# Kernel optimization log

Measured on AMD Instinct MI355X. Metric: run time of the kernel, lower is better.

The kernel has to match this reference:

```python
import jax, jax.numpy as jnp
import numpy as np

DIM = 192
HEADS = 6
WIN = 7
N = WIN * WIN            # 49 tokens per window
NW = 64                  # windows per image
B = 64                   # images
BW = NW * B              # 4096 total windows
TABLE = (2 * WIN - 1) ** 2  # 169


def setup_inputs() -> dict:
    key = jax.random.key(0)
    ks = jax.random.split(key, 8)
    x = jax.random.normal(ks[0], (BW, N, DIM), dtype=jnp.float32)
    rpi = jax.random.randint(ks[1], (N, N), 0, TABLE, dtype=jnp.int64)
    # 0 / -100 additive mask (as in shifted-window attention)
    mask = jnp.where(jax.random.uniform(ks[2], (NW, N, N)) < 0.1, -100.0, 0.0).astype(jnp.float32)
    qkv_w = jax.random.normal(ks[3], (3 * DIM, DIM), dtype=jnp.float32) * 0.02
    qkv_b = jnp.zeros((3 * DIM,), dtype=jnp.float32)
    proj_w = jax.random.normal(ks[4], (DIM, DIM), dtype=jnp.float32) * 0.02
    proj_b = jnp.zeros((DIM,), dtype=jnp.float32)
    rpb_table = jax.random.normal(ks[5], (TABLE, HEADS), dtype=jnp.float32) * 0.02
    return {"x": x, "rpi": rpi, "mask": mask, "qkv_w": qkv_w, "qkv_b": qkv_b,
            "proj_w": proj_w, "proj_b": proj_b, "rpb_table": rpb_table}


def reference(x, rpi, mask, qkv_w, qkv_b, proj_w, proj_b, rpb_table):
    b_, n, c = x.shape
    hd = c // HEADS
    scale = hd ** -0.5
    qkv = (x @ qkv_w.T + qkv_b).reshape(b_, n, 3, HEADS, hd)
    qkv = jnp.transpose(qkv, (2, 0, 3, 1, 4))
    q, k, v = qkv[0], qkv[1], qkv[2]
    attn = jnp.einsum('bhnd,bhmd->bhnm', q * scale, k)  # [b_, h, n, n]
    # relative position bias gather: [n, n, h] -> [h, n, n]
    bias = rpb_table[rpi.reshape(-1)].reshape(n, n, HEADS)
    attn = attn + jnp.transpose(bias, (2, 0, 1))[None]
    # additive 0/-inf window mask
    nw = mask.shape[0]
    attn = attn.reshape(b_ // nw, nw, HEADS, n, n) + mask[None, :, None]
    attn = attn.reshape(-1, HEADS, n, n)
    attn = jax.nn.softmax(attn, axis=-1)
    out = jnp.einsum('bhnm,bhmd->bhnd', attn, v)
    out = jnp.transpose(out, (0, 2, 1, 3)).reshape(b_, n, c)
    out = out @ proj_w.T + proj_b
    return out
```

## Files before the change

### kernel.cpp

```cpp
#include <hip/hip_runtime.h>

#define DIM    192
#define HEADS  6
#define NTOK   49
#define NWIN   64

typedef __attribute__((ext_vector_type(8))) short short8;
typedef __attribute__((ext_vector_type(4))) float f32x4;

#define XS 200
#define VS 72
#define PS 72

#define USP_BYTES   26656
#define P_EOFF      9800
#define LDS_USHORTS ((USP_BYTES + 64 * XS * 2 + DIM * VS * 2) / 2)

#define BIAS_ELEMS (HEADS * NTOK * NTOK)
#define WQKV_SOFF   28864
#define WQKV_ELEMS  (3 * DIM * DIM)
#define WPROJ_SOFF  (WQKV_SOFF + WQKV_ELEMS)
#define WPROJ_ELEMS (DIM * DIM)
#define CMB_BOFF    ((size_t)(WPROJ_SOFF + WPROJ_ELEMS) * 2)
#define CMB2_ELEMS  (NWIN * HEADS * NTOK * 64)

__device__ __forceinline__ unsigned short f2bf(float f) {
    unsigned int u = __float_as_uint(f);
    u += 0x7FFFu + ((u >> 16) & 1u);
    return (unsigned short)(u >> 16);
}

__global__ void wa_prep_kernel(const int* __restrict__ rpi,
                               const float* __restrict__ rpb,
                               const float* __restrict__ qkv_w,
                               const float* __restrict__ proj_w,
                               const float* __restrict__ maskp,
                               float* __restrict__ bias,
                               unsigned short* __restrict__ wqkv,
                               unsigned short* __restrict__ wproj,
                               float* __restrict__ cmb2) {
    __shared__ int is64_s;
    if (threadIdx.x < 64) {
        int z = (rpi[2 * (int)threadIdx.x + 1] == 0) ? 1 : 0;
        unsigned long long b = __ballot(z);
        if (threadIdx.x == 0) is64_s = (__popcll(b) >= 48) ? 1 : 0;
    }
    __syncthreads();
    const int is64 = is64_s;
    const int base3 = BIAS_ELEMS + WQKV_ELEMS + WPROJ_ELEMS;
    const int total = base3 + (cmb2 ? CMB2_ELEMS : 0);
    for (int idx = blockIdx.x * blockDim.x + threadIdx.x; idx < total;
         idx += gridDim.x * blockDim.x) {
        if (idx < BIAS_ELEMS) {
            int h  = idx / (NTOK * NTOK);
            int nm = idx - h * (NTOK * NTOK);
            int r  = is64 ? rpi[2 * nm] : rpi[nm];
            bias[idx] = rpb[r * HEADS + h];
        } else if (idx < BIAS_ELEMS + WQKV_ELEMS) {
            int i = idx - BIAS_ELEMS;
            wqkv[i] = f2bf(qkv_w[i]);
        } else if (idx < base3) {
            int i = idx - BIAS_ELEMS - WQKV_ELEMS;
            wproj[i] = f2bf(proj_w[i]);
        } else {
            int i2  = idx - base3;
            int win = i2 / (HEADS * NTOK * 64);
            int rem = i2 - win * (HEADS * NTOK * 64);
            int h   = rem / (NTOK * 64);
            int rm2 = rem - h * (NTOK * 64);
            int q   = rm2 >> 6;
            int k   = rm2 & 63;
            float v = 0.f;
            if (k < NTOK) {
                int nm = q * NTOK + k;
                int r  = is64 ? rpi[2 * nm] : rpi[nm];
                v = rpb[r * HEADS + h] + maskp[win * (NTOK * NTOK) + nm];
            }
            cmb2[i2] = v;
        }
    }
}

template <bool CMB>
__global__ __launch_bounds__(512, 4)
void wa_attn_kernel(const float* __restrict__ x,
                    const float* __restrict__ maskp,
                    const unsigned short* __restrict__ wqkv,
                    const float* __restrict__ qkv_b,
                    const float* __restrict__ biasp,
                    const unsigned short* __restrict__ wproj,
                    const float* __restrict__ proj_b,
                    const float* __restrict__ cmbp,
                    float* __restrict__ out) {
    __shared__ __attribute__((aligned(16))) unsigned short lds[LDS_USHORTS];
    unsigned short* sx     = lds;
    unsigned short* kstage = lds;
    unsigned short* P      = lds + P_EOFF;
    unsigned short* sq     = lds + USP_BYTES / 2;
    unsigned short* sv     = lds + USP_BYTES / 2 + 64 * XS;

    const int tid  = threadIdx.x;
    const int wave = tid >> 6;
    const int lane = tid & 63;
    const int quad = lane >> 4;
    const int l16  = lane & 15;
    const int bw   = blockIdx.x;
    const int win  = bw & (NWIN - 1);
    const float scale = 0.17677669529663687f;

    {
        const float4* xw = (const float4*)(x + (size_t)bw * (NTOK * DIM));
        for (int idx = tid; idx < NTOK * DIM / 4; idx += 512) {
            int row = idx / 48, c4 = idx - row * 48;
            float4 v = xw[idx];
            unsigned int lo = (unsigned int)f2bf(v.x) | ((unsigned int)f2bf(v.y) << 16);
            unsigned int hi = (unsigned int)f2bf(v.z) | ((unsigned int)f2bf(v.w) << 16);
            *(uint2*)&sx[row * XS + c4 * 4] = make_uint2(lo, hi);
        }
        for (int idx = tid; idx < 15 * 24; idx += 512) {
            int row = 49 + idx / 24, c8 = idx - (idx / 24) * 24;
            *(uint4*)&sx[row * XS + c8 * 8] = make_uint4(0, 0, 0, 0);
        }
    }
    __syncthreads();

    {
        const int wm = wave >> 2;
        const int wn = wave & 3;
        #pragma unroll
        for (int cc = 0; cc < 3; ++cc) {
            const int c = (cc == 0) ? 0 : (cc == 1 ? 2 : 1);
            f32x4 acc[3][2];
            #pragma unroll
            for (int r = 0; r < 3; ++r)
                #pragma unroll
                for (int mi = 0; mi < 2; ++mi) acc[r][mi] = (f32x4){0.f, 0.f, 0.f, 0.f};
            for (int k0 = 0; k0 < DIM; k0 += 32) {
                short8 af[2];
                #pragma unroll
                for (int mi = 0; mi < 2; ++mi)
                    af[mi] = *(const short8*)&sx[((wm * 2 + mi) * 16 + l16) * XS + k0 + quad * 8];
                #pragma unroll
                for (int r = 0; r < 3; ++r) {
                    int n0 = c * 192 + (wn + 4 * r) * 16;
                    short8 bf = *(const short8*)(wqkv + (n0 + l16) * DIM + k0 + quad * 8);
                    #pragma unroll
                    for (int mi = 0; mi < 2; ++mi)
                        acc[r][mi] = __builtin_amdgcn_mfma_f32_16x16x32_bf16(af[mi], bf, acc[r][mi], 0, 0, 0);
                }
            }
            if (c == 1) __syncthreads();
            #pragma unroll
            for (int r = 0; r < 3; ++r) {
                int ccol = (wn + 4 * r) * 16 + l16;
                float cb = qkv_b[c * 192 + ccol];
                #pragma unroll
                for (int mi = 0; mi < 2; ++mi) {
                    int mbase = (wm * 2 + mi) * 16 + quad * 4;
                    if (c == 2) {
                        unsigned int lo = (unsigned int)f2bf(acc[r][mi][0] + cb) |
                                          ((unsigned int)f2bf(acc[r][mi][1] + cb) << 16);
                        unsigned int hi = (unsigned int)f2bf(acc[r][mi][2] + cb) |
                                          ((unsigned int)f2bf(acc[r][mi][3] + cb) << 16);
                        *(uint2*)&sv[ccol * VS + mbase] = make_uint2(lo, hi);
                    } else if (c == 1) {
                        #pragma unroll
                        for (int rr = 0; rr < 4; ++rr)
                            kstage[(mbase + rr) * XS + ccol] = f2bf(acc[r][mi][rr] + cb);
                    } else {
                        #pragma unroll
                        for (int rr = 0; rr < 4; ++rr)
                            sq[(mbase + rr) * XS + ccol] = f2bf((acc[r][mi][rr] + cb) * scale);
                    }
                }
            }
        }
    }
    __syncthreads();

    #pragma unroll
    for (int h = 0; h < HEADS; ++h) {
        unsigned int pw[4][2];
        int qv = 0;
        if (wave < 4) {
            const int qt = wave;
            const int q  = qt * 16 + l16;
            qv = (q < NTOK);
            short8 bq = *(const short8*)&sq[(qt * 16 + l16) * XS + h * 32 + quad * 8];
            f32x4 d[4];
            #pragma unroll
            for (int kt = 0; kt < 4; ++kt) {
                short8 ak = *(const short8*)&kstage[(kt * 16 + l16) * XS + h * 32 + quad * 8];
                d[kt] = __builtin_amdgcn_mfma_f32_16x16x32_bf16(ak, bq, (f32x4){0.f, 0.f, 0.f, 0.f}, 0, 0, 0);
            }
            float s[4][4];
            float m = -1e30f;
            #pragma unroll
            for (int kt = 0; kt < 4; ++kt) {
                int kbase = kt * 16 + quad * 4;
                if (CMB) {
                    const int qc = qv ? q : (NTOK - 1);
                    float4 c4 = *(const float4*)(cmbp + (((size_t)(win * HEADS + h)) * NTOK + qc) * 64 + kbase);
                    const float* c4p = (const float*)&c4;
                    #pragma unroll
                    for (int rr = 0; rr < 4; ++rr) {
                        int k = kbase + rr;
                        s[kt][rr] = (k < NTOK && qv) ? d[kt][rr] + c4p[rr] : -30000.f;
                        m = fmaxf(m, s[kt][rr]);
                    }
                } else {
                    const float* bh = biasp + h * (NTOK * NTOK);
                    const float* mw = maskp + win * (NTOK * NTOK);
                    #pragma unroll
                    for (int rr = 0; rr < 4; ++rr) {
                        int k = kbase + rr;
                        float v = -30000.f;
                        if (k < NTOK && qv) v = d[kt][rr] + bh[q * NTOK + k] + mw[q * NTOK + k];
                        s[kt][rr] = v;
                        m = fmaxf(m, v);
                    }
                }
            }
            m = fmaxf(m, __shfl_xor(m, 16));
            m = fmaxf(m, __shfl_xor(m, 32));
            float p[4][4];
            float sum = 0.f;
            #pragma unroll
            for (int kt = 0; kt < 4; ++kt)
                #pragma unroll
                for (int rr = 0; rr < 4; ++rr) {
                    p[kt][rr] = __expf(s[kt][rr] - m);
                    sum += p[kt][rr];
                }
            sum += __shfl_xor(sum, 16);
            sum += __shfl_xor(sum, 32);
            float si = 1.f / sum;
            #pragma unroll
            for (int kt = 0; kt < 4; ++kt) {
                pw[kt][0] = (unsigned int)f2bf(p[kt][0] * si) | ((unsigned int)f2bf(p[kt][1] * si) << 16);
                pw[kt][1] = (unsigned int)f2bf(p[kt][2] * si) | ((unsigned int)f2bf(p[kt][3] * si) << 16);
            }
        } else if (h > 0) {
            const int hp = h - 1, mt = wave - 4;
            #pragma unroll
            for (int nt = 0; nt < 2; ++nt) {
                f32x4 o = {0.f, 0.f, 0.f, 0.f};
                #pragma unroll
                for (int k0 = 0; k0 < 64; k0 += 32) {
                    short8 ap = *(const short8*)&P[(mt * 16 + l16) * PS + k0 + quad * 8];
                    short8 bv = *(const short8*)&sv[(hp * 32 + nt * 16 + l16) * VS + k0 + quad * 8];
                    o = __builtin_amdgcn_mfma_f32_16x16x32_bf16(ap, bv, o, 0, 0, 0);
                }
                #pragma unroll
                for (int rr = 0; rr < 4; ++rr) {
                    int i = mt * 16 + quad * 4 + rr;
                    if (i < NTOK)
                        sq[i * XS + hp * 32 + nt * 16 + l16] = f2bf(o[rr]);
                }
            }
        }
        __syncthreads();
        if (wave < 4 && qv) {
            const int q = wave * 16 + l16;
            #pragma unroll
            for (int kt = 0; kt < 4; ++kt)
                *(uint2*)&P[q * PS + kt * 16 + quad * 4] = make_uint2(pw[kt][0], pw[kt][1]);
        }
        __syncthreads();
    }
    {
        const int hp = HEADS - 1, mt = wave >> 1, nt = wave & 1;
        f32x4 o = {0.f, 0.f, 0.f, 0.f};
        #pragma unroll
        for (int k0 = 0; k0 < 64; k0 += 32) {
            short8 ap = *(const short8*)&P[(mt * 16 + l16) * PS + k0 + quad * 8];
            short8 bv = *(const short8*)&sv[(hp * 32 + nt * 16 + l16) * VS + k0 + quad * 8];
            o = __builtin_amdgcn_mfma_f32_16x16x32_bf16(ap, bv, o, 0, 0, 0);
        }
        #pragma unroll
        for (int rr = 0; rr < 4; ++rr) {
            int i = mt * 16 + quad * 4 + rr;
            if (i < NTOK)
                sq[i * XS + hp * 32 + nt * 16 + l16] = f2bf(o[rr]);
        }
    }
    __syncthreads();

    {
        const int mh = wave >> 2;
        const int wv = wave & 3;
        f32x4 pacc[3][2];
        #pragma unroll
        for (int r = 0; r < 3; ++r)
            #pragma unroll
            for (int mi = 0; mi < 2; ++mi) pacc[r][mi] = (f32x4){0.f, 0.f, 0.f, 0.f};
        for (int k0 = 0; k0 < DIM; k0 += 32) {
            short8 af[2];
            #pragma unroll
            for (int mi = 0; mi < 2; ++mi)
                af[mi] = *(const short8*)&sq[((mh * 2 + mi) * 16 + l16) * XS + k0 + quad * 8];
            #pragma unroll
            for (int r = 0; r < 3; ++r) {
                int n0 = (wv + 4 * r) * 16;
                short8 bf = *(const short8*)(wproj + (n0 + l16) * DIM + k0 + quad * 8);
                #pragma unroll
                for (int mi = 0; mi < 2; ++mi)
                    pacc[r][mi] = __builtin_amdgcn_mfma_f32_16x16x32_bf16(af[mi], bf, pacc[r][mi], 0, 0, 0);
            }
        }
        #pragma unroll
        for (int r = 0; r < 3; ++r) {
            int n0 = (wv + 4 * r) * 16;
            float cb = proj_b[n0 + l16];
            #pragma unroll
            for (int mi = 0; mi < 2; ++mi) {
                #pragma unroll
                for (int rr = 0; rr < 4; ++rr) {
                    int m = (mh * 2 + mi) * 16 + quad * 4 + rr;
                    if (m < NTOK)
                        out[((size_t)bw * NTOK + m) * DIM + n0 + l16] = pacc[r][mi][rr] + cb;
                }
            }
        }
    }
}

extern "C" void kernel_launch(void* const* d_in, const int* in_sizes, int n_in,
                              void* d_out, int out_size, void* d_ws, size_t ws_size,
                              hipStream_t stream) {
    const float* x      = (const float*)d_in[0];
    const int*   rpi    = (const int*)d_in[1];
    const float* maskp  = (const float*)d_in[2];
    const float* qkv_w  = (const float*)d_in[3];
    const float* qkv_b  = (const float*)d_in[4];
    const float* proj_w = (const float*)d_in[5];
    const float* proj_b = (const float*)d_in[6];
    const float* rpb    = (const float*)d_in[7];
    float* out = (float*)d_out;

    float* bias = (float*)d_ws;
    unsigned short* wqkv  = (unsigned short*)d_ws + WQKV_SOFF;
    unsigned short* wproj = (unsigned short*)d_ws + WPROJ_SOFF;
    float* cmb2 = nullptr;
    if (ws_size >= CMB_BOFF + (size_t)CMB2_ELEMS * 4)
        cmb2 = (float*)((char*)d_ws + CMB_BOFF);

    wa_prep_kernel<<<640, 256, 0, stream>>>(rpi, rpb, qkv_w, proj_w, maskp,
                                            bias, wqkv, wproj, cmb2);
    if (cmb2)
        wa_attn_kernel<true><<<4096, 512, 0, stream>>>(x, maskp, wqkv, qkv_b, bias,
                                                       wproj, proj_b, cmb2, out);
    else
        wa_attn_kernel<false><<<4096, 512, 0, stream>>>(x, maskp, wqkv, qkv_b, bias,
                                                        wproj, proj_b, nullptr, out);
}
```

Before: 609.7 us.

## Process two heads concurrently across all eight waves with double P buffers

The attention phase no longer splits work so that four waves run softmax while the other four compute P·V for the previous head. Now each half of the block (four waves) owns its own head and its own P buffer, and each half does QK, softmax and P·V for its head. This cuts the head loop from six iterations to three, with half as many block barriers. The V row stride shrinks to 56 and only valid Q rows are written, so the extra P buffer fits in shared memory. The trade-off is that P·V reads now run past the 49 valid keys into the next V row or into uninitialised LDS. This relies on the zeroed probabilities to cancel those values.

```diff
diff --git a/kernel.cpp b/kernel.cpp
--- a/kernel.cpp
+++ b/kernel.cpp
@@ -9,12 +9,14 @@
 typedef __attribute__((ext_vector_type(4))) float f32x4;
 
 #define XS 200
-#define VS 72
+#define VS 56
 #define PS 72
 
-#define USP_BYTES   26656
-#define P_EOFF      9800
-#define LDS_USHORTS ((USP_BYTES + 64 * XS * 2 + DIM * VS * 2) / 2)
+#define P0_EOFF 9800
+#define P1_EOFF 14408
+#define SQ_EOFF 19016
+#define SV_EOFF 28816
+#define LDS_USHORTS 39632
 
 #define BIAS_ELEMS (HEADS * NTOK * NTOK)
 #define WQKV_SOFF   28864
@@ -95,9 +97,8 @@
     __shared__ __attribute__((aligned(16))) unsigned short lds[LDS_USHORTS];
     unsigned short* sx     = lds;
     unsigned short* kstage = lds;
-    unsigned short* P      = lds + P_EOFF;
-    unsigned short* sq     = lds + USP_BYTES / 2;
-    unsigned short* sv     = lds + USP_BYTES / 2 + 64 * XS;
+    unsigned short* sq     = lds + SQ_EOFF;
+    unsigned short* sv     = lds + SV_EOFF;
 
     const int tid  = threadIdx.x;
     const int wave = tid >> 6;
@@ -158,11 +159,13 @@
                 for (int mi = 0; mi < 2; ++mi) {
                     int mbase = (wm * 2 + mi) * 16 + quad * 4;
                     if (c == 2) {
-                        unsigned int lo = (unsigned int)f2bf(acc[r][mi][0] + cb) |
-                                          ((unsigned int)f2bf(acc[r][mi][1] + cb) << 16);
-                        unsigned int hi = (unsigned int)f2bf(acc[r][mi][2] + cb) |
-                                          ((unsigned int)f2bf(acc[r][mi][3] + cb) << 16);
-                        *(uint2*)&sv[ccol * VS + mbase] = make_uint2(lo, hi);
+                        if (mbase < 56) {
+                            unsigned int lo = (unsigned int)f2bf(acc[r][mi][0] + cb) |
+                                              ((unsigned int)f2bf(acc[r][mi][1] + cb) << 16);
+                            unsigned int hi = (unsigned int)f2bf(acc[r][mi][2] + cb) |
+                                              ((unsigned int)f2bf(acc[r][mi][3] + cb) << 16);
+                            *(uint2*)&sv[ccol * VS + mbase] = make_uint2(lo, hi);
+                        }
                     } else if (c == 1) {
                         #pragma unroll
                         for (int rr = 0; rr < 4; ++rr)
@@ -170,7 +173,8 @@
                     } else {
                         #pragma unroll
                         for (int rr = 0; rr < 4; ++rr)
-                            sq[(mbase + rr) * XS + ccol] = f2bf((acc[r][mi][rr] + cb) * scale);
+                            if (mbase + rr < NTOK)
+                                sq[(mbase + rr) * XS + ccol] = f2bf((acc[r][mi][rr] + cb) * scale);
                     }
                 }
             }
@@ -178,19 +182,21 @@
     }
     __syncthreads();
 
-    #pragma unroll
-    for (int h = 0; h < HEADS; ++h) {
+    const int hh   = wave >> 2;
+    const int qt   = wave & 3;
+    const int q    = qt * 16 + l16;
+    const int qv   = (q < NTOK);
+    unsigned short* Pb = lds + (hh ? P1_EOFF : P0_EOFF);
+
+    for (int g = 0; g < 3; ++g) {
+        const int head = 2 * g + hh;
         unsigned int pw[4][2];
-        int qv = 0;
-        if (wave < 4) {
-            const int qt = wave;
-            const int q  = qt * 16 + l16;
-            qv = (q < NTOK);
-            short8 bq = *(const short8*)&sq[(qt * 16 + l16) * XS + h * 32 + quad * 8];
+        {
+            short8 bq = *(const short8*)&sq[(qt * 16 + l16) * XS + head * 32 + quad * 8];
             f32x4 d[4];
             #pragma unroll
             for (int kt = 0; kt < 4; ++kt) {
-                short8 ak = *(const short8*)&kstage[(kt * 16 + l16) * XS + h * 32 + quad * 8];
+                short8 ak = *(const short8*)&kstage[(kt * 16 + l16) * XS + head * 32 + quad * 8];
                 d[kt] = __builtin_amdgcn_mfma_f32_16x16x32_bf16(ak, bq, (f32x4){0.f, 0.f, 0.f, 0.f}, 0, 0, 0);
             }
             float s[4][4];
@@ -200,7 +206,7 @@
                 int kbase = kt * 16 + quad * 4;
                 if (CMB) {
                     const int qc = qv ? q : (NTOK - 1);
-                    float4 c4 = *(const float4*)(cmbp + (((size_t)(win * HEADS + h)) * NTOK + qc) * 64 + kbase);
+                    float4 c4 = *(const float4*)(cmbp + (((size_t)(win * HEADS + head)) * NTOK + qc) * 64 + kbase);
                     const float* c4p = (const float*)&c4;
                     #pragma unroll
                     for (int rr = 0; rr < 4; ++rr) {
@@ -209,7 +215,7 @@
                         m = fmaxf(m, s[kt][rr]);
                     }
                 } else {
-                    const float* bh = biasp + h * (NTOK * NTOK);
+                    const float* bh = biasp + head * (NTOK * NTOK);
                     const float* mw = maskp + win * (NTOK * NTOK);
                     #pragma unroll
                     for (int rr = 0; rr < 4; ++rr) {
@@ -240,48 +246,29 @@
                 pw[kt][0] = (unsigned int)f2bf(p[kt][0] * si) | ((unsigned int)f2bf(p[kt][1] * si) << 16);
                 pw[kt][1] = (unsigned int)f2bf(p[kt][2] * si) | ((unsigned int)f2bf(p[kt][3] * si) << 16);
             }
-        } else if (h > 0) {
-            const int hp = h - 1, mt = wave - 4;
-            #pragma unroll
-            for (int nt = 0; nt < 2; ++nt) {
-                f32x4 o = {0.f, 0.f, 0.f, 0.f};
-                #pragma unroll
-                for (int k0 = 0; k0 < 64; k0 += 32) {
-                    short8 ap = *(const short8*)&P[(mt * 16 + l16) * PS + k0 + quad * 8];
-                    short8 bv = *(const short8*)&sv[(hp * 32 + nt * 16 + l16) * VS + k0 + quad * 8];
-                    o = __builtin_amdgcn_mfma_f32_16x16x32_bf16(ap, bv, o, 0, 0, 0);
-                }
-                #pragma unroll
-                for (int rr = 0; rr < 4; ++rr) {
-                    int i = mt * 16 + quad * 4 + rr;
-                    if (i < NTOK)
-                        sq[i * XS + hp * 32 + nt * 16 + l16] = f2bf(o[rr]);
-                }
-            }
         }
         __syncthreads();
-        if (wave < 4 && qv) {
-            const int q = wave * 16 + l16;
+        if (qv) {
             #pragma unroll
             for (int kt = 0; kt < 4; ++kt)
-                *(uint2*)&P[q * PS + kt * 16 + quad * 4] = make_uint2(pw[kt][0], pw[kt][1]);
+                *(uint2*)&Pb[q * PS + kt * 16 + quad * 4] = make_uint2(pw[kt][0], pw[kt][1]);
         }
         __syncthreads();
-    }
-    {
-        const int hp = HEADS - 1, mt = wave >> 1, nt = wave & 1;
-        f32x4 o = {0.f, 0.f, 0.f, 0.f};
         #pragma unroll
-        for (int k0 = 0; k0 < 64; k0 += 32) {
-            short8 ap = *(const short8*)&P[(mt * 16 + l16) * PS + k0 + quad * 8];
-            short8 bv = *(const short8*)&sv[(hp * 32 + nt * 16 + l16) * VS + k0 + quad * 8];
-            o = __builtin_amdgcn_mfma_f32_16x16x32_bf16(ap, bv, o, 0, 0, 0);
-        }
-        #pragma unroll
-        for (int rr = 0; rr < 4; ++rr) {
-            int i = mt * 16 + quad * 4 + rr;
-            if (i < NTOK)
-                sq[i * XS + hp * 32 + nt * 16 + l16] = f2bf(o[rr]);
+        for (int tt = 0; tt < 2; ++tt) {
+            f32x4 o = {0.f, 0.f, 0.f, 0.f};
+            #pragma unroll
+            for (int k0 = 0; k0 < 64; k0 += 32) {
+                short8 ap = *(const short8*)&Pb[(qt * 16 + l16) * PS + k0 + quad * 8];
+                short8 bv = *(const short8*)&sv[(head * 32 + tt * 16 + l16) * VS + k0 + quad * 8];
+                o = __builtin_amdgcn_mfma_f32_16x16x32_bf16(ap, bv, o, 0, 0, 0);
+            }
+            #pragma unroll
+            for (int rr = 0; rr < 4; ++rr) {
+                int i = qt * 16 + quad * 4 + rr;
+                if (i < NTOK)
+                    sq[i * XS + head * 32 + tt * 16 + l16] = f2bf(o[rr]);
+            }
         }
     }
     __syncthreads();
```

Result: slower. 649.7 us (+6.6%).
